# Optimization experiments

Hardware: AMD Instinct MI355X
Metric: run time of the kernel (lower is better)

Reference implementation:

```python
import jax, jax.numpy as jnp
import numpy as np

N_HEAD, QK_DIM, V_DIM = 8, 32, 32
INNER = N_HEAD * V_DIM  # 256
D_MODEL = 256
N_VAR = 2
NEG = -1e9
LN_EPS = 1e-5


def irregular_rope(q, t):
    # q: [BN, L, H, D], t: [BN, L]
    D = q.shape[-1]
    inv_freq = 1.0 / (10000.0 ** (jnp.arange(0, D, 2, dtype=jnp.float32) / D))  # [D/2]
    ang = t[:, :, None, None] * inv_freq[None, None, None, :]  # [BN, L, 1, D/2]
    cos, sin = jnp.cos(ang), jnp.sin(ang)
    q1, q2 = q[..., 0::2], q[..., 1::2]
    out = jnp.stack([q1 * cos - q2 * sin, q1 * sin + q2 * cos], axis=-1)
    return out.reshape(q.shape)


def layernorm(x, g, b):
    mu = jnp.mean(x, axis=-1, keepdims=True)
    var = jnp.mean((x - mu) ** 2, axis=-1, keepdims=True)
    return (x - mu) * jax.lax.rsqrt(var + LN_EPS) * g + b


def setup_inputs() -> dict:
    key = jax.random.key(0)
    ks = jax.random.split(key, 14)
    B, PN, PL = 16, 64, 128
    x = jax.random.normal(ks[0], (B, PN, PL, N_VAR), dtype=jnp.float32)
    t = jnp.sort(jax.random.uniform(ks[1], (B, PN, PL + 1), dtype=jnp.float32) * 100.0, axis=-1)
    mask = jax.random.randint(ks[2], (B, PN, PL + 1), 0, 2, dtype=jnp.int32)
    mask = mask.at[..., 0].set(1)  # emb token never masked
    s = 0.05
    return {
        "x": x, "t": t, "mask": mask,
        "emb_token": jnp.zeros((1, 1, 1, N_VAR), dtype=jnp.float32),
        "Wq": jax.random.normal(ks[3], (N_VAR, N_HEAD * QK_DIM), dtype=jnp.float32) * s,
        "Wk": jax.random.normal(ks[4], (N_VAR, N_HEAD * QK_DIM), dtype=jnp.float32) * s,
        "Wv": jax.random.normal(ks[5], (N_VAR, N_HEAD * V_DIM), dtype=jnp.float32) * s,
        "Wo": jax.random.normal(ks[6], (INNER, D_MODEL), dtype=jnp.float32) * s,
        "ln_g": jnp.ones((INNER,), dtype=jnp.float32),
        "ln_b": jnp.zeros((INNER,), dtype=jnp.float32),
        "W1": jax.random.normal(ks[7], (INNER, 4 * INNER), dtype=jnp.float32) * s,
        "b1": jnp.zeros((4 * INNER,), dtype=jnp.float32),
        "W2": jax.random.normal(ks[8], (4 * INNER, INNER), dtype=jnp.float32) * s,
        "b2": jnp.zeros((INNER,), dtype=jnp.float32),
    }


def reference(x, t, mask, emb_token, Wq, Wk, Wv, Wo, ln_g, ln_b, W1, b1, W2, b2):
    B, PN, PL, _ = x.shape
    L = PL + 1
    BN = B * PN
    emb = jnp.broadcast_to(emb_token, (B, PN, 1, N_VAR))
    _x = jnp.concatenate([emb, x], axis=2)  # [B, PN, L, 2]
    Q = (_x @ Wq).reshape(BN, L, N_HEAD, QK_DIM)
    K = (_x @ Wk).reshape(BN, L, N_HEAD, QK_DIM)
    V = (_x @ Wv).reshape(BN, L, N_HEAD, V_DIM)
    tt = t.reshape(BN, L)
    Q = irregular_rope(Q, tt)
    K = irregular_rope(K, tt)
    # attention: [BN, H, L, L]
    scores = jnp.einsum('blhd,bmhd->bhlm', Q, K) / jnp.sqrt(jnp.float32(QK_DIM))
    m = mask.reshape(BN, L).astype(jnp.float32)
    mask_mat = (m[:, :, None] * m[:, None, :])[:, None, :, :]  # [BN,1,L,L]
    scores = jnp.where(mask_mat > 0, scores, NEG)
    attn = jax.nn.softmax(scores, axis=-1)
    ctx = jnp.einsum('bhlm,bmhd->blhd', attn, V)  # [BN, L, H, Dv]
    last = ctx[:, 0].reshape(B, PN, INNER)  # emb-token output
    h = layernorm(last, ln_g, ln_b)
    h = jax.nn.relu(h @ W1 + b1) @ W2 + b2
    last = last + h
    return last @ Wo  # [B, PN, D_MODEL]
```

## Files before the change

kernel.cpp:

```cpp
#include <hip/hip_runtime.h>
#include <math.h>

#define LSEQ   129
#define PLEN   128
#define NHEAD  8
#define DHEAD  32
#define INNER  256
#define HID    1024

typedef _Float16 h2 __attribute__((ext_vector_type(2)));
typedef _Float16 h8 __attribute__((ext_vector_type(8)));

__device__ __forceinline__ float fdot2(h2 a, h2 b, float c) {
#if __has_builtin(__builtin_amdgcn_fdot2)
    return __builtin_amdgcn_fdot2(a, b, c, false);
#else
    return c + (float)a.x * (float)b.x + (float)a.y * (float)b.y;
#endif
}

__device__ __forceinline__ float dot8(h8 a, h8 b, float c) {
    h2 a0 = __builtin_shufflevector(a, a, 0, 1);
    h2 a1 = __builtin_shufflevector(a, a, 2, 3);
    h2 a2 = __builtin_shufflevector(a, a, 4, 5);
    h2 a3 = __builtin_shufflevector(a, a, 6, 7);
    h2 b0 = __builtin_shufflevector(b, b, 0, 1);
    h2 b1 = __builtin_shufflevector(b, b, 2, 3);
    h2 b2 = __builtin_shufflevector(b, b, 4, 5);
    h2 b3 = __builtin_shufflevector(b, b, 6, 7);
    c = fdot2(a0, b0, c);
    c = fdot2(a1, b1, c);
    c = fdot2(a2, b2, c);
    c = fdot2(a3, b3, c);
    return c;
}

__global__ __launch_bounds__(256) void attn_kernel(
    const float* __restrict__ x,
    const float* __restrict__ t,
    const int*   __restrict__ mask,
    const float* __restrict__ emb,
    const float* __restrict__ Wq,
    const float* __restrict__ Wk,
    const float* __restrict__ Wv,
    const float* __restrict__ W1,
    const float* __restrict__ W2,
    const float* __restrict__ Wo,
    float*       __restrict__ last,
    h8*          __restrict__ W1o,
    h8*          __restrict__ W2o,
    h8*          __restrict__ Woo)
{
    const int bn  = blockIdx.x;
    const int tid = threadIdx.x;

    {
        int g = bn * 256 + tid;
        if (g < 73728) {
            h8 v;
            if (g < 32768) {
                int c8 = g >> 10, j = g & 1023;
                const float* src = W1 + (8 * c8) * HID + j;
#pragma unroll
                for (int i = 0; i < 8; ++i) v[i] = (_Float16)src[i * HID];
                W1o[g] = v;
            } else if (g < 65536) {
                int l = g - 32768;
                int c8 = l >> 8, o = l & 255;
                const float* src = W2 + (8 * c8) * INNER + o;
#pragma unroll
                for (int i = 0; i < 8; ++i) v[i] = (_Float16)src[i * INNER];
                W2o[l] = v;
            } else {
                int l = g - 65536;
                int c8 = l >> 8, o = l & 255;
                const float* src = Wo + (8 * c8) * INNER + o;
#pragma unroll
                for (int i = 0; i < 8; ++i) v[i] = (_Float16)src[i * INNER];
                Woo[l] = v;
            }
        }
    }

    __shared__ float2 cs_s[16][132];
    __shared__ float2 x_s[132];
    __shared__ float4 ab_s[8][16];
    __shared__ float  sc_s[8][132];
    __shared__ int    mask_s[132];
    __shared__ float  hstat_s[8][3];

    const float* tb = t + bn * LSEQ;
    const float t0  = tb[0];
    const float e0 = emb[0], e1 = emb[1];

    if (tid < 130) {
        float2 v;
        if (tid == 0)        v = make_float2(e0, e1);
        else if (tid <= 128) v = ((const float2*)(x + bn * PLEN * 2))[tid - 1];
        else                 v = make_float2(0.f, 0.f);
        x_s[tid] = v;
    }
    if (tid < 129) mask_s[tid] = mask[bn * LSEQ + tid];

    for (int i = tid; i < 129 * 16; i += 256) {
        int m = i >> 4, j = i & 15;
        float invf = exp2f(-(float)j * 0.8304820237218407f);
        float sv, cv;
        __sincosf((tb[m] - t0) * invf, &sv, &cv);
        cs_s[j][m] = make_float2(cv, sv);
    }

    if (tid < 128) {
        int h = tid >> 4, j = tid & 15;
        int ce = h * 32 + 2 * j, co = ce + 1;
        float qe = e0 * Wq[ce] + e1 * Wq[256 + ce];
        float qo = e0 * Wq[co] + e1 * Wq[256 + co];
        float k0e = Wk[ce], k0o = Wk[co];
        float k1e = Wk[256 + ce], k1o = Wk[256 + co];
        const float sc = 0.17677669529663687f;
        ab_s[h][j] = make_float4((qe * k0e + qo * k0o) * sc,
                                 (qo * k0e - qe * k0o) * sc,
                                 (qe * k1e + qo * k1o) * sc,
                                 (qo * k1e - qe * k1o) * sc);
    }
    __syncthreads();

    const int lane = tid & 63;
    const int wv   = tid >> 6;
    const int h    = wv * 2 + (lane >> 5);
    const int l32  = lane & 31;

    float4 ab[16];
#pragma unroll
    for (int j = 0; j < 16; ++j) ab[j] = ab_s[h][j];

#pragma unroll
    for (int k = 0; k < 5; ++k) {
        int m = l32 + 32 * k;
        if (m < 129) {
            float2 xv = x_s[m];
            float accA = 0.f, accB = 0.f;
#pragma unroll
            for (int j = 0; j < 16; ++j) {
                float2 cs = cs_s[j][m];
                accA = fmaf(cs.x, ab[j].x, accA);
                accA = fmaf(cs.y, ab[j].y, accA);
                accB = fmaf(cs.x, ab[j].z, accB);
                accB = fmaf(cs.y, ab[j].w, accB);
            }
            sc_s[h][m] = accA * xv.x + accB * xv.y;
        }
    }
    __syncthreads();

    const int mask0 = mask_s[0];
    float se[5];
    float M = -1e30f;
#pragma unroll
    for (int k = 0; k < 5; ++k) {
        int m = l32 + 32 * k;
        float s;
        if (m < 129) {
            s = sc_s[h][m];
            if (mask0 == 0)          s = 0.f;
            else if (mask_s[m] == 0) s = -1e9f;
        } else s = -1e30f;
        se[k] = s;
        M = fmaxf(M, s);
    }
#pragma unroll
    for (int off = 16; off >= 1; off >>= 1) M = fmaxf(M, __shfl_xor(M, off, 64));

    float den = 0.f, S0 = 0.f, S1 = 0.f;
#pragma unroll
    for (int k = 0; k < 5; ++k) {
        int m = l32 + 32 * k;
        if (m < 129) {
            float e = __expf(se[k] - M);
            float2 xv = x_s[m];
            den += e;
            S0 = fmaf(e, xv.x, S0);
            S1 = fmaf(e, xv.y, S1);
        }
    }
#pragma unroll
    for (int off = 16; off >= 1; off >>= 1) {
        den += __shfl_xor(den, off, 64);
        S0  += __shfl_xor(S0,  off, 64);
        S1  += __shfl_xor(S1,  off, 64);
    }
    if (l32 == 0) {
        hstat_s[h][0] = den; hstat_s[h][1] = S0; hstat_s[h][2] = S1;
    }
    __syncthreads();

    {
        int hh = tid >> 5;
        float inv = 1.f / hstat_s[hh][0];
        last[bn * 256 + tid] =
            (hstat_s[hh][1] * Wv[tid] + hstat_s[hh][2] * Wv[256 + tid]) * inv;
    }
}

__global__ __launch_bounds__(1024) void mlp_kernel(
    const float* __restrict__ last,
    const float* __restrict__ ln_g,
    const float* __restrict__ ln_b,
    const h8*    __restrict__ W1o,
    const float* __restrict__ b1,
    const h8*    __restrict__ W2o,
    const float* __restrict__ b2,
    const h8*    __restrict__ Woo,
    float*       __restrict__ out)
{
    const int tid = threadIdx.x;
    const int r0  = blockIdx.x * 4;
    const int rg  = tid >> 8;
    const int ch  = tid & 255;

    __shared__ alignas(16) _Float16 h_h[4][INNER];
    __shared__ alignas(16) _Float16 y_h[4][HID];
    __shared__ alignas(16) _Float16 r_h[4][INNER];
    __shared__ float p_s[4][4][INNER];
    __shared__ float red_s[16][2];

    float xv = last[(r0 + rg) * INNER + ch];

    float s1 = xv, s2 = xv * xv;
#pragma unroll
    for (int off = 32; off >= 1; off >>= 1) {
        s1 += __shfl_xor(s1, off, 64);
        s2 += __shfl_xor(s2, off, 64);
    }
    const int wave = tid >> 6;
    if ((tid & 63) == 0) { red_s[wave][0] = s1; red_s[wave][1] = s2; }
    __syncthreads();

    {
        float t1 = red_s[4 * rg + 0][0] + red_s[4 * rg + 1][0] +
                   red_s[4 * rg + 2][0] + red_s[4 * rg + 3][0];
        float t2 = red_s[4 * rg + 0][1] + red_s[4 * rg + 1][1] +
                   red_s[4 * rg + 2][1] + red_s[4 * rg + 3][1];
        float mu  = t1 * (1.f / 256.f);
        float var = t2 * (1.f / 256.f) - mu * mu;
        float rs  = rsqrtf(var + 1e-5f);
        h_h[rg][ch] = (_Float16)((xv - mu) * rs * ln_g[ch] + ln_b[ch]);
    }
    __syncthreads();

    {
        float a0, a1v, a2v, a3;
        a0 = a1v = a2v = a3 = b1[tid];
        const h8* w = W1o + tid;
#pragma unroll 8
        for (int c8 = 0; c8 < 32; ++c8) {
            h8 wv = w[c8 * HID];
            h8 h0 = *(const h8*)&h_h[0][c8 * 8];
            h8 h1 = *(const h8*)&h_h[1][c8 * 8];
            h8 hh2 = *(const h8*)&h_h[2][c8 * 8];
            h8 h3 = *(const h8*)&h_h[3][c8 * 8];
            a0  = dot8(h0, wv, a0);
            a1v = dot8(h1, wv, a1v);
            a2v = dot8(hh2, wv, a2v);
            a3  = dot8(h3, wv, a3);
        }
        y_h[0][tid] = (_Float16)fmaxf(a0, 0.f);
        y_h[1][tid] = (_Float16)fmaxf(a1v, 0.f);
        y_h[2][tid] = (_Float16)fmaxf(a2v, 0.f);
        y_h[3][tid] = (_Float16)fmaxf(a3, 0.f);
    }
    __syncthreads();

    {
        float a0 = 0.f, a1v = 0.f, a2v = 0.f, a3 = 0.f;
        const h8* w = W2o + rg * 32 * INNER + ch;
#pragma unroll 8
        for (int i = 0; i < 32; ++i) {
            int c8 = rg * 32 + i;
            h8 wv = w[i * INNER];
            h8 y0 = *(const h8*)&y_h[0][c8 * 8];
            h8 y1 = *(const h8*)&y_h[1][c8 * 8];
            h8 y2 = *(const h8*)&y_h[2][c8 * 8];
            h8 y3 = *(const h8*)&y_h[3][c8 * 8];
            a0  = dot8(y0, wv, a0);
            a1v = dot8(y1, wv, a1v);
            a2v = dot8(y2, wv, a2v);
            a3  = dot8(y3, wv, a3);
        }
        p_s[rg][0][ch] = a0;
        p_s[rg][1][ch] = a1v;
        p_s[rg][2][ch] = a2v;
        p_s[rg][3][ch] = a3;
    }
    __syncthreads();

    {
        float rv = xv + b2[ch] +
                   p_s[0][rg][ch] + p_s[1][rg][ch] +
                   p_s[2][rg][ch] + p_s[3][rg][ch];
        r_h[rg][ch] = (_Float16)rv;
    }
    __syncthreads();

    {
        float a0 = 0.f, a1v = 0.f, a2v = 0.f, a3 = 0.f;
        const h8* w = Woo + rg * 8 * INNER + ch;
#pragma unroll
        for (int i = 0; i < 8; ++i) {
            int c8 = rg * 8 + i;
            h8 wv = w[i * INNER];
            h8 v0 = *(const h8*)&r_h[0][c8 * 8];
            h8 v1 = *(const h8*)&r_h[1][c8 * 8];
            h8 v2 = *(const h8*)&r_h[2][c8 * 8];
            h8 v3 = *(const h8*)&r_h[3][c8 * 8];
            a0  = dot8(v0, wv, a0);
            a1v = dot8(v1, wv, a1v);
            a2v = dot8(v2, wv, a2v);
            a3  = dot8(v3, wv, a3);
        }
        p_s[rg][0][ch] = a0;
        p_s[rg][1][ch] = a1v;
        p_s[rg][2][ch] = a2v;
        p_s[rg][3][ch] = a3;
    }
    __syncthreads();

    out[(r0 + rg) * INNER + ch] = p_s[0][rg][ch] + p_s[1][rg][ch] +
                                  p_s[2][rg][ch] + p_s[3][rg][ch];
}

extern "C" void kernel_launch(void* const* d_in, const int* in_sizes, int n_in,
                              void* d_out, int out_size, void* d_ws, size_t ws_size,
                              hipStream_t stream) {
    const float* x    = (const float*)d_in[0];
    const float* t    = (const float*)d_in[1];
    const int*   mask = (const int*)  d_in[2];
    const float* emb  = (const float*)d_in[3];
    const float* Wq   = (const float*)d_in[4];
    const float* Wk   = (const float*)d_in[5];
    const float* Wv   = (const float*)d_in[6];
    const float* Wo   = (const float*)d_in[7];
    const float* ln_g = (const float*)d_in[8];
    const float* ln_b = (const float*)d_in[9];
    const float* W1   = (const float*)d_in[10];
    const float* b1   = (const float*)d_in[11];
    const float* W2   = (const float*)d_in[12];
    const float* b2   = (const float*)d_in[13];
    float* out = (float*)d_out;

    const int BN = in_sizes[1] / LSEQ;

    char* ws = (char*)d_ws;
    float* last_ws = (float*)ws;
    h8* W1o = (h8*)(ws + (1u << 20));
    h8* W2o = (h8*)(ws + (1u << 20) + (512u << 10));
    h8* Woo = (h8*)(ws + (2u << 20));

    attn_kernel<<<BN, 256, 0, stream>>>(x, t, mask, emb, Wq, Wk, Wv,
                                        W1, W2, Wo, last_ws, W1o, W2o, Woo);
    mlp_kernel<<<BN / 4, 1024, 0, stream>>>(last_ws, ln_g, ln_b, W1o, b1,
                                            W2o, b2, Woo, out);
}
```

Before: 107.7 us.

## Rewrite MLP kernel with MFMA 16x16x32 f16 over 16-row tiles

Replaces the fdot2-based MLP (four rows per block) with a matrix-core version that handles sixteen rows per block using 16x16x32 f16 MFMA instructions. LayerNorm now runs per wavefront with float4 loads, and the shared-memory arrays are padded to reduce bank conflicts. Each fetched weight vector is now reused across sixteen rows instead of four, which cuts weight traffic and replaces scalar dot-product work with matrix instructions. The grid shrinks by a factor of four, leaving only 64 blocks, which may underfill the GPU.

```diff
diff --git a/kernel.cpp b/kernel.cpp
--- a/kernel.cpp
+++ b/kernel.cpp
@@ -9,31 +9,9 @@
 #define HID    1024
 
 typedef _Float16 h2 __attribute__((ext_vector_type(2)));
+typedef _Float16 h4 __attribute__((ext_vector_type(4)));
 typedef _Float16 h8 __attribute__((ext_vector_type(8)));
-
-__device__ __forceinline__ float fdot2(h2 a, h2 b, float c) {
-#if __has_builtin(__builtin_amdgcn_fdot2)
-    return __builtin_amdgcn_fdot2(a, b, c, false);
-#else
-    return c + (float)a.x * (float)b.x + (float)a.y * (float)b.y;
-#endif
-}
-
-__device__ __forceinline__ float dot8(h8 a, h8 b, float c) {
-    h2 a0 = __builtin_shufflevector(a, a, 0, 1);
-    h2 a1 = __builtin_shufflevector(a, a, 2, 3);
-    h2 a2 = __builtin_shufflevector(a, a, 4, 5);
-    h2 a3 = __builtin_shufflevector(a, a, 6, 7);
-    h2 b0 = __builtin_shufflevector(b, b, 0, 1);
-    h2 b1 = __builtin_shufflevector(b, b, 2, 3);
-    h2 b2 = __builtin_shufflevector(b, b, 4, 5);
-    h2 b3 = __builtin_shufflevector(b, b, 6, 7);
-    c = fdot2(a0, b0, c);
-    c = fdot2(a1, b1, c);
-    c = fdot2(a2, b2, c);
-    c = fdot2(a3, b3, c);
-    return c;
-}
+typedef float    f32x4 __attribute__((ext_vector_type(4)));
 
 __global__ __launch_bounds__(256) void attn_kernel(
     const float* __restrict__ x,
@@ -213,120 +191,103 @@
     const h8*    __restrict__ Woo,
     float*       __restrict__ out)
 {
-    const int tid = threadIdx.x;
-    const int r0  = blockIdx.x * 4;
-    const int rg  = tid >> 8;
-    const int ch  = tid & 255;
-
-    __shared__ alignas(16) _Float16 h_h[4][INNER];
-    __shared__ alignas(16) _Float16 y_h[4][HID];
-    __shared__ alignas(16) _Float16 r_h[4][INNER];
-    __shared__ float p_s[4][4][INNER];
-    __shared__ float red_s[16][2];
-
-    float xv = last[(r0 + rg) * INNER + ch];
-
-    float s1 = xv, s2 = xv * xv;
-#pragma unroll
-    for (int off = 32; off >= 1; off >>= 1) {
-        s1 += __shfl_xor(s1, off, 64);
-        s2 += __shfl_xor(s2, off, 64);
-    }
-    const int wave = tid >> 6;
-    if ((tid & 63) == 0) { red_s[wave][0] = s1; red_s[wave][1] = s2; }
-    __syncthreads();
-
-    {
-        float t1 = red_s[4 * rg + 0][0] + red_s[4 * rg + 1][0] +
-                   red_s[4 * rg + 2][0] + red_s[4 * rg + 3][0];
-        float t2 = red_s[4 * rg + 0][1] + red_s[4 * rg + 1][1] +
-                   red_s[4 * rg + 2][1] + red_s[4 * rg + 3][1];
-        float mu  = t1 * (1.f / 256.f);
-        float var = t2 * (1.f / 256.f) - mu * mu;
+    const int tid  = threadIdx.x;
+    const int w    = tid >> 6;
+    const int lane = tid & 63;
+    const int g    = lane >> 4;
+    const int lr   = lane & 15;
+    const int r0   = blockIdx.x * 16;
+
+    __shared__ alignas(16) _Float16 h_h[16][264];
+    __shared__ alignas(16) _Float16 y_h[16][1032];
+    __shared__ alignas(16) _Float16 r_h[16][264];
+    __shared__ alignas(16) float    last_s[16][260];
+
+    {
+        float4 v = ((const float4*)(last + (r0 + w) * INNER))[lane];
+        *(float4*)&last_s[w][lane * 4] = v;
+        float s1 = v.x + v.y + v.z + v.w;
+        float s2 = v.x * v.x + v.y * v.y + v.z * v.z + v.w * v.w;
+#pragma unroll
+        for (int off = 32; off >= 1; off >>= 1) {
+            s1 += __shfl_xor(s1, off, 64);
+            s2 += __shfl_xor(s2, off, 64);
+        }
+        float mu  = s1 * (1.f / 256.f);
+        float var = s2 * (1.f / 256.f) - mu * mu;
         float rs  = rsqrtf(var + 1e-5f);
-        h_h[rg][ch] = (_Float16)((xv - mu) * rs * ln_g[ch] + ln_b[ch]);
-    }
-    __syncthreads();
-
-    {
-        float a0, a1v, a2v, a3;
-        a0 = a1v = a2v = a3 = b1[tid];
-        const h8* w = W1o + tid;
-#pragma unroll 8
-        for (int c8 = 0; c8 < 32; ++c8) {
-            h8 wv = w[c8 * HID];
-            h8 h0 = *(const h8*)&h_h[0][c8 * 8];
-            h8 h1 = *(const h8*)&h_h[1][c8 * 8];
-            h8 hh2 = *(const h8*)&h_h[2][c8 * 8];
-            h8 h3 = *(const h8*)&h_h[3][c8 * 8];
-            a0  = dot8(h0, wv, a0);
-            a1v = dot8(h1, wv, a1v);
-            a2v = dot8(hh2, wv, a2v);
-            a3  = dot8(h3, wv, a3);
-        }
-        y_h[0][tid] = (_Float16)fmaxf(a0, 0.f);
-        y_h[1][tid] = (_Float16)fmaxf(a1v, 0.f);
-        y_h[2][tid] = (_Float16)fmaxf(a2v, 0.f);
-        y_h[3][tid] = (_Float16)fmaxf(a3, 0.f);
-    }
-    __syncthreads();
-
-    {
-        float a0 = 0.f, a1v = 0.f, a2v = 0.f, a3 = 0.f;
-        const h8* w = W2o + rg * 32 * INNER + ch;
-#pragma unroll 8
-        for (int i = 0; i < 32; ++i) {
-            int c8 = rg * 32 + i;
-            h8 wv = w[i * INNER];
-            h8 y0 = *(const h8*)&y_h[0][c8 * 8];
-            h8 y1 = *(const h8*)&y_h[1][c8 * 8];
-            h8 y2 = *(const h8*)&y_h[2][c8 * 8];
-            h8 y3 = *(const h8*)&y_h[3][c8 * 8];
-            a0  = dot8(y0, wv, a0);
-            a1v = dot8(y1, wv, a1v);
-            a2v = dot8(y2, wv, a2v);
-            a3  = dot8(y3, wv, a3);
-        }
-        p_s[rg][0][ch] = a0;
-        p_s[rg][1][ch] = a1v;
-        p_s[rg][2][ch] = a2v;
-        p_s[rg][3][ch] = a3;
-    }
-    __syncthreads();
-
-    {
-        float rv = xv + b2[ch] +
-                   p_s[0][rg][ch] + p_s[1][rg][ch] +
-                   p_s[2][rg][ch] + p_s[3][rg][ch];
-        r_h[rg][ch] = (_Float16)rv;
-    }
-    __syncthreads();
-
-    {
-        float a0 = 0.f, a1v = 0.f, a2v = 0.f, a3 = 0.f;
-        const h8* w = Woo + rg * 8 * INNER + ch;
-#pragma unroll
-        for (int i = 0; i < 8; ++i) {
-            int c8 = rg * 8 + i;
-            h8 wv = w[i * INNER];
-            h8 v0 = *(const h8*)&r_h[0][c8 * 8];
-            h8 v1 = *(const h8*)&r_h[1][c8 * 8];
-            h8 v2 = *(const h8*)&r_h[2][c8 * 8];
-            h8 v3 = *(const h8*)&r_h[3][c8 * 8];
-            a0  = dot8(v0, wv, a0);
-            a1v = dot8(v1, wv, a1v);
-            a2v = dot8(v2, wv, a2v);
-            a3  = dot8(v3, wv, a3);
-        }
-        p_s[rg][0][ch] = a0;
-        p_s[rg][1][ch] = a1v;
-        p_s[rg][2][ch] = a2v;
-        p_s[rg][3][ch] = a3;
-    }
-    __syncthreads();
-
-    out[(r0 + rg) * INNER + ch] = p_s[0][rg][ch] + p_s[1][rg][ch] +
-                                  p_s[2][rg][ch] + p_s[3][rg][ch];
+        float4 gv = ((const float4*)ln_g)[lane];
+        float4 bv = ((const float4*)ln_b)[lane];
+        h4 hv;
+        hv[0] = (_Float16)((v.x - mu) * rs * gv.x + bv.x);
+        hv[1] = (_Float16)((v.y - mu) * rs * gv.y + bv.y);
+        hv[2] = (_Float16)((v.z - mu) * rs * gv.z + bv.z);
+        hv[3] = (_Float16)((v.w - mu) * rs * gv.w + bv.w);
+        *(h4*)&h_h[w][lane * 4] = hv;
+    }
+    __syncthreads();
+
+    {
+        f32x4 acc0 = {0.f, 0.f, 0.f, 0.f};
+        f32x4 acc1 = {0.f, 0.f, 0.f, 0.f};
+        f32x4 acc2 = {0.f, 0.f, 0.f, 0.f};
+        f32x4 acc3 = {0.f, 0.f, 0.f, 0.f};
+        const int cbase = 64 * w + lr;
+        const h8* wp = W1o + g * HID + cbase;
+#pragma unroll 2
+        for (int k8 = 0; k8 < 32; k8 += 4) {
+            h8 a = *(const h8*)&h_h[lr][(k8 + g) * 8];
+            const h8* wk = wp + k8 * HID;
+            acc0 = __builtin_amdgcn_mfma_f32_16x16x32_f16(a, wk[0],  acc0, 0, 0, 0);
+            acc1 = __builtin_amdgcn_mfma_f32_16x16x32_f16(a, wk[16], acc1, 0, 0, 0);
+            acc2 = __builtin_amdgcn_mfma_f32_16x16x32_f16(a, wk[32], acc2, 0, 0, 0);
+            acc3 = __builtin_amdgcn_mfma_f32_16x16x32_f16(a, wk[48], acc3, 0, 0, 0);
+        }
+        const float b10 = b1[cbase];
+        const float b11 = b1[cbase + 16];
+        const float b12 = b1[cbase + 32];
+        const float b13 = b1[cbase + 48];
+#pragma unroll
+        for (int r = 0; r < 4; ++r) {
+            int row = g * 4 + r;
+            y_h[row][cbase]      = (_Float16)fmaxf(acc0[r] + b10, 0.f);
+            y_h[row][cbase + 16] = (_Float16)fmaxf(acc1[r] + b11, 0.f);
+            y_h[row][cbase + 32] = (_Float16)fmaxf(acc2[r] + b12, 0.f);
+            y_h[row][cbase + 48] = (_Float16)fmaxf(acc3[r] + b13, 0.f);
+        }
+    }
+    __syncthreads();
+
+    const int col = 16 * w + lr;
+    {
+        f32x4 acc = {0.f, 0.f, 0.f, 0.f};
+        const h8* wp = W2o + g * INNER + col;
+#pragma unroll 4
+        for (int k8 = 0; k8 < 128; k8 += 4) {
+            h8 a = *(const h8*)&y_h[lr][(k8 + g) * 8];
+            acc = __builtin_amdgcn_mfma_f32_16x16x32_f16(a, wp[k8 * INNER], acc, 0, 0, 0);
+        }
+        const float bb = b2[col];
+#pragma unroll
+        for (int r = 0; r < 4; ++r) {
+            int row = g * 4 + r;
+            r_h[row][col] = (_Float16)(last_s[row][col] + bb + acc[r]);
+        }
+    }
+    __syncthreads();
+
+    {
+        f32x4 acc = {0.f, 0.f, 0.f, 0.f};
+        const h8* wp = Woo + g * INNER + col;
+#pragma unroll
+        for (int k8 = 0; k8 < 32; k8 += 4) {
+            h8 a = *(const h8*)&r_h[lr][(k8 + g) * 8];
+            acc = __builtin_amdgcn_mfma_f32_16x16x32_f16(a, wp[k8 * INNER], acc, 0, 0, 0);
+        }
+#pragma unroll
+        for (int r = 0; r < 4; ++r)
+            out[(r0 + g * 4 + r) * INNER + col] = acc[r];
+    }
 }
 
 extern "C" void kernel_launch(void* const* d_in, const int* in_sizes, int n_in,
@@ -358,6 +319,6 @@
 
     attn_kernel<<<BN, 256, 0, stream>>>(x, t, mask, emb, Wq, Wk, Wv,
                                         W1, W2, Wo, last_ws, W1o, W2o, Woo);
-    mlp_kernel<<<BN / 4, 1024, 0, stream>>>(last_ws, ln_g, ln_b, W1o, b1,
-                                            W2o, b2, Woo, out);
+    mlp_kernel<<<BN / 16, 1024, 0, stream>>>(last_ws, ln_g, ln_b, W1o, b1,
+                                             W2o, b2, Woo, out);
 }
```

New measurement: 105.7 us. Within noise of the previous version (-1.9%).
